# Performance work log

Hardware: AMD Instinct MI355X
Metric: run time of the kernel (lower is better)

Reference implementation:

```python
import jax, jax.numpy as jnp
import numpy as np

N = 100000   # nodes
E = 800000   # directed edges (before self loops)
D = 300      # feature dim (SGConv(300, 300))


def setup_inputs() -> dict:
    key = jax.random.key(0)
    k1, k2, k3, k4 = jax.random.split(key, 4)
    x = jax.random.normal(k1, (N, D), dtype=jnp.float32)
    edge_index = jax.random.randint(k2, (2, E), 0, N, dtype=jnp.int32)
    # Linear(300, 300) params (kaiming-uniform-ish scale)
    bound = 1.0 / np.sqrt(D)
    W = jax.random.uniform(k3, (D, D), jnp.float32, -bound, bound)
    b = jax.random.uniform(k4, (D,), jnp.float32, -bound, bound)
    return {"x": x, "edge_index": edge_index, "W": W, "b": b}


def _sgc_forward(x, edge_index, W, b):
    n = x.shape[0]
    # --- GCN normalization with self loops (PyG SGConv defaults, K=1) ---
    loop = jnp.arange(n, dtype=edge_index.dtype)
    row = jnp.concatenate([edge_index[0], loop])   # source nodes
    col = jnp.concatenate([edge_index[1], loop])   # target nodes (aggregation index)
    deg = jax.ops.segment_sum(jnp.ones_like(col, dtype=x.dtype), col, num_segments=n)
    dinv = jnp.where(deg > 0, jax.lax.rsqrt(deg), 0.0)
    w = dinv[row] * dinv[col]                      # [E+N] edge norm
    # --- one hop of sparse propagation: out[c] += w * x[r] ---
    h = jax.ops.segment_sum(x[row] * w[:, None], col, num_segments=n)  # [N, D]
    # --- linear map ---
    h = h @ W.T + b
    # --- relu (dropout p=0 is identity) ---
    h = jax.nn.relu(h)
    # --- F.normalize: row-wise L2 with eps clamp ---
    norm = jnp.linalg.norm(h, axis=-1, keepdims=True)
    return h / jnp.maximum(norm, 1e-12)


def reference(x, edge_index, W, b):
    return _sgc_forward(x, edge_index, W, b)
```

## Files before the change

kernel.cpp:

```cpp
#include <hip/hip_runtime.h>
#include <hip/hip_bf16.h>
#include <stdint.h>

#define D 300
#define KP 320
#define JP 304
#define NT 19

typedef __hip_bfloat16 bf16;
typedef __bf16 bf16x8 __attribute__((ext_vector_type(8)));
typedef unsigned short us8 __attribute__((ext_vector_type(8)));
typedef float f32x4 __attribute__((ext_vector_type(4)));

static __device__ __forceinline__ unsigned short f2bu(float f) {
    bf16 h = __float2bfloat16(f);
    return *reinterpret_cast<unsigned short*>(&h);
}
static __device__ __forceinline__ float bulo(unsigned int u) {
    return __uint_as_float(u << 16);
}
static __device__ __forceinline__ float buhi(unsigned int u) {
    return __uint_as_float(u & 0xffff0000u);
}
static __device__ __forceinline__ void gload_lds16(const void* g, void* l) {
    __builtin_amdgcn_global_load_lds(
        (const __attribute__((address_space(1))) unsigned int*)g,
        (__attribute__((address_space(3))) unsigned int*)l, 16, 0, 0);
}

__global__ void k_count(const int* __restrict__ col, int* __restrict__ deg, int e) {
    int i = blockIdx.x * 256 + threadIdx.x;
    if (i < e) atomicAdd(&deg[col[i]], 1);
}

__global__ void k_scanA(const int* __restrict__ deg, int* __restrict__ ex,
                        float* __restrict__ dinv, int* __restrict__ bsum, int n) {
    __shared__ int sh[256];
    int tid = threadIdx.x;
    int base = blockIdx.x * 1024 + tid * 4;
    int v[4]; int s = 0;
#pragma unroll
    for (int t = 0; t < 4; t++) {
        int i = base + t;
        v[t] = (i < n) ? deg[i] : 0;
        if (i < n) dinv[i] = rsqrtf((float)(v[t] + 1));
        s += v[t];
    }
    sh[tid] = s;
    __syncthreads();
    for (int off = 1; off < 256; off <<= 1) {
        int t = (tid >= off) ? sh[tid - off] : 0;
        __syncthreads();
        sh[tid] += t;
        __syncthreads();
    }
    int excl = sh[tid] - s;
#pragma unroll
    for (int t = 0; t < 4; t++) {
        int i = base + t;
        if (i < n) ex[i] = excl;
        excl += v[t];
    }
    if (tid == 255) bsum[blockIdx.x] = sh[255];
}

__global__ void k_scanB(const int* __restrict__ bsum, int* __restrict__ bexc, int nb) {
    __shared__ int sh[256];
    int tid = threadIdx.x;
    int s = (tid < nb) ? bsum[tid] : 0;
    sh[tid] = s;
    __syncthreads();
    for (int off = 1; off < 256; off <<= 1) {
        int t = (tid >= off) ? sh[tid - off] : 0;
        __syncthreads();
        sh[tid] += t;
        __syncthreads();
    }
    bexc[tid] = sh[tid] - s;
}

__global__ void k_scanC(int* __restrict__ starts, const int* __restrict__ bexc, int n) {
    int i = blockIdx.x * 256 + threadIdx.x;
    if (i < n) starts[i] += bexc[i >> 10];
}

__global__ void k_fill(const int* __restrict__ ei, const float* __restrict__ dinv,
                       const int* __restrict__ starts, int* __restrict__ cursor,
                       uint2* __restrict__ edges, int e) {
    int i = blockIdx.x * 256 + threadIdx.x;
    if (i < e) {
        int r = ei[i];
        int c = ei[e + i];
        int p = atomicAdd(&cursor[c], 1);
        edges[starts[c] + p] = make_uint2((unsigned int)r,
                                          __float_as_uint(dinv[r] * dinv[c]));
    }
}

__global__ void k_twb(const float* __restrict__ W, unsigned short* __restrict__ wbp) {
    int idx = blockIdx.x * 256 + threadIdx.x;
    if (idx < JP * KP) {
        int j = idx / KP, k = idx - j * KP;
        wbp[idx] = (j < D && k < D) ? f2bu(W[j * D + k]) : (unsigned short)0;
    }
}

__global__ __launch_bounds__(256)
void k_zmm(const float* __restrict__ x, const unsigned short* __restrict__ wbp,
           unsigned short* __restrict__ zb, int n) {
    __shared__ unsigned short Wsh[JP * 32];
    __shared__ float Ash[2048];
    int tid = threadIdx.x;
    int lane = tid & 63, wid = tid >> 6;
    int r0 = blockIdx.x * 64 + wid * 16;
    int lrow = lane & 15, kg = lane >> 4;

    int goff[5];
#pragma unroll
    for (int j = 0; j < 5; j++) {
        int i = wid + 4 * j;
        if (i < 19) {
            int u = i * 64 + lane;
            int kgs = u / 304;
            int rs  = u - kgs * 304;
            goff[j] = rs * (KP * 2) + kgs * 16;
        }
    }
    const char* wb = (const char*)wbp;

    const float* ab[2];
    int thr[2];
#pragma unroll
    for (int j = 0; j < 2; j++) {
        int u = tid + 256 * j;
        int kgs = u >> 7, rem = u & 127, row = rem >> 1, half = rem & 1;
        int rg = blockIdx.x * 64 + row; if (rg >= n) rg = n - 1;
        int off = kgs * 8 + half * 4;
        ab[j] = x + (size_t)rg * D + off;
        thr[j] = 296 - off;
    }

    f32x4 acc[NT];
#pragma unroll
    for (int t = 0; t < NT; t++) acc[t] = f32x4{0.f, 0.f, 0.f, 0.f};

    const float* afp = &Ash[kg * 512 + (wid * 16 + lrow) * 8];
    const unsigned short* bbase = &Wsh[0] + (kg * 304 + lrow) * 8;

    for (int kk = 0; kk < KP / 32; kk++) {
#pragma unroll
        for (int j = 0; j < 5; j++) {
            int i = wid + 4 * j;
            if (i < 19) gload_lds16(wb + goff[j] + kk * 64, (char*)&Wsh[0] + i * 1024);
        }
        {
            const float* s0 = (kk * 32 <= thr[0]) ? ab[0] + kk * 32 : x;
            const float* s1 = (kk * 32 <= thr[1]) ? ab[1] + kk * 32 : x;
            gload_lds16(s0, (char*)&Ash[0] + wid * 1024);
            gload_lds16(s1, (char*)&Ash[0] + 4096 + wid * 1024);
        }
        __syncthreads();

        float4 pa = *(const float4*)afp;
        float4 pb = *(const float4*)(afp + 4);
        us8 au;
        au[0] = f2bu(pa.x); au[1] = f2bu(pa.y); au[2] = f2bu(pa.z); au[3] = f2bu(pa.w);
        au[4] = f2bu(pb.x); au[5] = f2bu(pb.y); au[6] = f2bu(pb.z); au[7] = f2bu(pb.w);
        bf16x8 av = __builtin_bit_cast(bf16x8, au);
#pragma unroll
        for (int t = 0; t < NT; t++) {
            bf16x8 bv = __builtin_bit_cast(bf16x8, *(const us8*)(bbase + t * 128));
            acc[t] = __builtin_amdgcn_mfma_f32_16x16x32_bf16(av, bv, acc[t], 0, 0, 0);
        }
        __syncthreads();
    }

#pragma unroll
    for (int r = 0; r < 4; r++) {
        int g0 = r0 + kg * 4 + r;
        if (g0 < n) {
            unsigned short* zp0 = zb + (size_t)g0 * JP;
#pragma unroll
            for (int t = 0; t < NT; t++) {
                int j = t * 16 + lrow;
                zp0[j] = f2bu(acc[t][r]);
            }
        }
    }
}

__global__ void k_zgather(const uint2* __restrict__ zb2, const uint2* __restrict__ edges,
                          const int* __restrict__ starts, const int* __restrict__ deg,
                          const float* __restrict__ dinv, const float* __restrict__ bias,
                          float* __restrict__ out, int n) {
    int w = (blockIdx.x * blockDim.x + threadIdx.x) >> 6;
    if (w >= n) return;
    int lane = threadIdx.x & 63;
    int s = starts[w];
    int cnt = deg[w];
    float dc = dinv[w];
    const bool p2 = lane < 12;
    float a0 = 0.f, a1 = 0.f, a2 = 0.f, a3 = 0.f;
    float a4 = 0.f, a5 = 0.f, a6 = 0.f, a7 = 0.f;
    const uint2 Z = make_uint2(0u, 0u);

#define GACC(ua, ub, wgt)                                                     \
    {                                                                         \
        a0 += (wgt) * bulo((ua).x); a1 += (wgt) * buhi((ua).x);               \
        a2 += (wgt) * bulo((ua).y); a3 += (wgt) * buhi((ua).y);               \
        a4 += (wgt) * bulo((ub).x); a5 += (wgt) * buhi((ub).x);               \
        a6 += (wgt) * bulo((ub).y); a7 += (wgt) * buhi((ub).y);               \
    }

    int t = 0;
    for (; t + 4 <= cnt; t += 4) {
        uint2 e0 = edges[s + t],     e1 = edges[s + t + 1];
        uint2 e2 = edges[s + t + 2], e3 = edges[s + t + 3];
        const uint2* q0 = zb2 + (size_t)e0.x * 76 + lane;
        const uint2* q1 = zb2 + (size_t)e1.x * 76 + lane;
        const uint2* q2 = zb2 + (size_t)e2.x * 76 + lane;
        const uint2* q3 = zb2 + (size_t)e3.x * 76 + lane;
        uint2 u0a = q0[0], u1a = q1[0], u2a = q2[0], u3a = q3[0];
        uint2 u0b = p2 ? q0[64] : Z;
        uint2 u1b = p2 ? q1[64] : Z;
        uint2 u2b = p2 ? q2[64] : Z;
        uint2 u3b = p2 ? q3[64] : Z;
        float w0 = __uint_as_float(e0.y), w1 = __uint_as_float(e1.y);
        float w2 = __uint_as_float(e2.y), w3 = __uint_as_float(e3.y);
        GACC(u0a, u0b, w0);
        GACC(u1a, u1b, w1);
        GACC(u2a, u2b, w2);
        GACC(u3a, u3b, w3);
    }
    for (; t < cnt; t++) {
        uint2 ed = edges[s + t];
        float wg = __uint_as_float(ed.y);
        const uint2* q = zb2 + (size_t)ed.x * 76 + lane;
        uint2 ua = q[0];
        uint2 ub = p2 ? q[64] : Z;
        GACC(ua, ub, wg);
    }
    {
        float sw = dc * dc;
        const uint2* q = zb2 + (size_t)w * 76 + lane;
        uint2 ua = q[0];
        uint2 ub = p2 ? q[64] : Z;
        GACC(ua, ub, sw);
    }
#undef GACC

    float4 b0 = *(const float4*)(bias + 4 * lane);
    float4 b1 = {0.f, 0.f, 0.f, 0.f};
    const bool wr2 = lane < 11;
    if (wr2) b1 = *(const float4*)(bias + 256 + 4 * lane);
    float v0 = fmaxf(a0 + b0.x, 0.f), v1 = fmaxf(a1 + b0.y, 0.f);
    float v2 = fmaxf(a2 + b0.z, 0.f), v3 = fmaxf(a3 + b0.w, 0.f);
    float v4 = fmaxf(a4 + b1.x, 0.f), v5 = fmaxf(a5 + b1.y, 0.f);
    float v6 = fmaxf(a6 + b1.z, 0.f), v7 = fmaxf(a7 + b1.w, 0.f);
    float sq = v0 * v0 + v1 * v1 + v2 * v2 + v3 * v3
             + v4 * v4 + v5 * v5 + v6 * v6 + v7 * v7;
    sq += __shfl_xor(sq, 1);
    sq += __shfl_xor(sq, 2);
    sq += __shfl_xor(sq, 4);
    sq += __shfl_xor(sq, 8);
    sq += __shfl_xor(sq, 16);
    sq += __shfl_xor(sq, 32);
    float sc = rsqrtf(fmaxf(sq, 1e-24f));

    float* op = out + (size_t)w * D;
    f32x4 o0 = {v0 * sc, v1 * sc, v2 * sc, v3 * sc};
    __builtin_nontemporal_store(o0, (f32x4*)(op + 4 * lane));
    if (wr2) {
        f32x4 o1 = {v4 * sc, v5 * sc, v6 * sc, v7 * sc};
        __builtin_nontemporal_store(o1, (f32x4*)(op + 256 + 4 * lane));
    }
}

extern "C" void kernel_launch(void* const* d_in, const int* in_sizes, int n_in,
                              void* d_out, int out_size, void* d_ws, size_t ws_size,
                              hipStream_t stream) {
    const float* x  = (const float*)d_in[0];
    const int*   ei = (const int*)d_in[1];
    const float* W  = (const float*)d_in[2];
    const float* b  = (const float*)d_in[3];
    float* out = (float*)d_out;
    int n = in_sizes[0] / D;
    int e = in_sizes[1] / 2;

    char* p = (char*)d_ws;
    unsigned short* zb = (unsigned short*)p; p += (size_t)n * JP * 2;
    int* deg = (int*)p;         p += (size_t)n * 4;
    int* cursor = (int*)p;      p += (size_t)n * 4;
    float* dinv = (float*)p;    p += (size_t)n * 4;
    int* starts = (int*)p;      p += (size_t)n * 4;
    p = (char*)(((uintptr_t)p + 15) & ~(uintptr_t)15);
    uint2* edges = (uint2*)p;   p += (size_t)e * 8;
    int* bsum = (int*)p;        p += 256 * 4;
    int* bexc = (int*)p;        p += 256 * 4;
    p = (char*)(((uintptr_t)p + 15) & ~(uintptr_t)15);
    unsigned short* wbp = (unsigned short*)p; p += (size_t)JP * KP * 2;

    int nb = (n + 1023) / 1024;

    (void)hipMemsetAsync(deg, 0, (size_t)n * 8, stream);
    k_count<<<(e + 255) / 256, 256, 0, stream>>>(ei + e, deg, e);
    k_scanA<<<nb, 256, 0, stream>>>(deg, starts, dinv, bsum, n);
    k_scanB<<<1, 256, 0, stream>>>(bsum, bexc, nb);
    k_scanC<<<(n + 255) / 256, 256, 0, stream>>>(starts, bexc, n);
    k_fill <<<(e + 255) / 256, 256, 0, stream>>>(ei, dinv, starts, cursor, edges, e);
    k_twb  <<<(JP * KP + 255) / 256, 256, 0, stream>>>(W, wbp);
    k_zmm  <<<(n + 63) / 64, 256, 0, stream>>>(x, wbp, zb, n);
    k_zgather<<<(n + 3) / 4, 256, 0, stream>>>((const uint2*)zb, edges, starts, deg,
                                               dinv, b, out, n);
}
```

Measured before the change: 277.0 us.

## Double-buffer W tiles in LDS and prefetch x directly into registers

```diff
diff --git a/kernel.cpp b/kernel.cpp
--- a/kernel.cpp
+++ b/kernel.cpp
@@ -100,7 +100,13 @@
 __global__ void k_twb(const float* __restrict__ W, unsigned short* __restrict__ wbp) {
     int idx = blockIdx.x * 256 + threadIdx.x;
     if (idx < JP * KP) {
-        int j = idx / KP, k = idx - j * KP;
+        int i = idx & 7;
+        int lrow = (idx >> 3) & 15;
+        int kg = (idx >> 7) & 3;
+        int q = idx >> 9;
+        int kk = q / 19, t = q - kk * 19;
+        int j = t * 16 + lrow;
+        int k = kk * 32 + kg * 8 + i;
         wbp[idx] = (j < D && k < D) ? f2bu(W[j * D + k]) : (unsigned short)0;
     }
 }
@@ -108,71 +114,64 @@
 __global__ __launch_bounds__(256)
 void k_zmm(const float* __restrict__ x, const unsigned short* __restrict__ wbp,
            unsigned short* __restrict__ zb, int n) {
-    __shared__ unsigned short Wsh[JP * 32];
-    __shared__ float Ash[2048];
+    __shared__ unsigned short Wsh[2][JP * 32];
     int tid = threadIdx.x;
     int lane = tid & 63, wid = tid >> 6;
     int r0 = blockIdx.x * 64 + wid * 16;
     int lrow = lane & 15, kg = lane >> 4;
 
-    int goff[5];
+    int soff[5];
 #pragma unroll
     for (int j = 0; j < 5; j++) {
         int i = wid + 4 * j;
-        if (i < 19) {
-            int u = i * 64 + lane;
-            int kgs = u / 304;
-            int rs  = u - kgs * 304;
-            goff[j] = rs * (KP * 2) + kgs * 16;
+        soff[j] = (i < 19) ? (i * 1024 + lane * 16) : -1;
+    }
+    const char* wb = (const char*)wbp;
+
+    int arow = r0 + lrow; if (arow >= n) arow = n - 1;
+    const float* xr = x + (size_t)arow * D;
+
+    f32x4 acc[NT];
+#pragma unroll
+    for (int t = 0; t < NT; t++) acc[t] = f32x4{0.f, 0.f, 0.f, 0.f};
+
+    float4 pa, pb;
+    {
+        int c = kg * 8;
+        pa = *(const float4*)(xr + c);
+        pb = *(const float4*)(xr + c + 4);
+#pragma unroll
+        for (int j = 0; j < 5; j++)
+            if (soff[j] >= 0) gload_lds16(wb + soff[j], (char*)&Wsh[0][0] + soff[j]);
+    }
+    __syncthreads();
+
+    for (int kk = 0; kk < KP / 32; kk++) {
+        float4 na, nb2;
+        if (kk < KP / 32 - 1) {
+            int c = (kk + 1) * 32 + kg * 8;
+            int clo = (c <= 296) ? c : 0;
+            int chi = (c <= 292) ? c + 4 : 0;
+            na  = *(const float4*)(xr + clo);
+            nb2 = *(const float4*)(xr + chi);
+            int gof = (kk + 1) * (JP * 64);
+            char* lbase = (char*)&Wsh[(kk + 1) & 1][0];
+#pragma unroll
+            for (int j = 0; j < 5; j++)
+                if (soff[j] >= 0) gload_lds16(wb + gof + soff[j], lbase + soff[j]);
         }
-    }
-    const char* wb = (const char*)wbp;
-
-    const float* ab[2];
-    int thr[2];
-#pragma unroll
-    for (int j = 0; j < 2; j++) {
-        int u = tid + 256 * j;
-        int kgs = u >> 7, rem = u & 127, row = rem >> 1, half = rem & 1;
-        int rg = blockIdx.x * 64 + row; if (rg >= n) rg = n - 1;
-        int off = kgs * 8 + half * 4;
-        ab[j] = x + (size_t)rg * D + off;
-        thr[j] = 296 - off;
-    }
-
-    f32x4 acc[NT];
-#pragma unroll
-    for (int t = 0; t < NT; t++) acc[t] = f32x4{0.f, 0.f, 0.f, 0.f};
-
-    const float* afp = &Ash[kg * 512 + (wid * 16 + lrow) * 8];
-    const unsigned short* bbase = &Wsh[0] + (kg * 304 + lrow) * 8;
-
-    for (int kk = 0; kk < KP / 32; kk++) {
-#pragma unroll
-        for (int j = 0; j < 5; j++) {
-            int i = wid + 4 * j;
-            if (i < 19) gload_lds16(wb + goff[j] + kk * 64, (char*)&Wsh[0] + i * 1024);
-        }
-        {
-            const float* s0 = (kk * 32 <= thr[0]) ? ab[0] + kk * 32 : x;
-            const float* s1 = (kk * 32 <= thr[1]) ? ab[1] + kk * 32 : x;
-            gload_lds16(s0, (char*)&Ash[0] + wid * 1024);
-            gload_lds16(s1, (char*)&Ash[0] + 4096 + wid * 1024);
-        }
-        __syncthreads();
-
-        float4 pa = *(const float4*)afp;
-        float4 pb = *(const float4*)(afp + 4);
         us8 au;
         au[0] = f2bu(pa.x); au[1] = f2bu(pa.y); au[2] = f2bu(pa.z); au[3] = f2bu(pa.w);
         au[4] = f2bu(pb.x); au[5] = f2bu(pb.y); au[6] = f2bu(pb.z); au[7] = f2bu(pb.w);
         bf16x8 av = __builtin_bit_cast(bf16x8, au);
+        const unsigned short* bbase = &Wsh[kk & 1][0] + lane * 8;
 #pragma unroll
         for (int t = 0; t < NT; t++) {
-            bf16x8 bv = __builtin_bit_cast(bf16x8, *(const us8*)(bbase + t * 128));
+            bf16x8 bv = __builtin_bit_cast(bf16x8, *(const us8*)(bbase + t * 512));
             acc[t] = __builtin_amdgcn_mfma_f32_16x16x32_bf16(av, bv, acc[t], 0, 0, 0);
         }
         __syncthreads();
+        pa = na; pb = nb2;
     }
 
 #pragma unroll
```

Measured after the change: 238.1 us. 1.16x faster.
